# Optimization experiments

Hardware: AMD Instinct MI355X
Metric: run time of the kernel (lower is better)

## Reference

```python
import jax, jax.numpy as jnp
import numpy as np

B, H, S, D = 4, 16, 2048, 64


def setup_inputs() -> dict:
    key = jax.random.key(0)
    kq, kk, kv = jax.random.split(key, 3)
    q = jax.random.normal(kq, (B, H, S, D), dtype=jnp.float32)
    k = jax.random.normal(kk, (B, H, S, D), dtype=jnp.float32)
    v = jax.random.normal(kv, (B, H, S, D), dtype=jnp.float32)
    # causal mask, broadcastable over batch/heads (True = keep)
    mask = jnp.tril(jnp.ones((S, S), dtype=bool))[None, None, :, :]
    return {"q": q, "k": k, "v": v, "mask": mask}


def reference(q, k, v, mask):
    d_k = q.shape[-1]
    # [..., q, k] scores with full materialization, as in the original
    scores = jnp.einsum("bhqd,bhkd->bhqk", q, k) / jnp.sqrt(jnp.float32(d_k))
    scores = jnp.where(mask, scores, jnp.float32(-jnp.inf))
    attn = jax.nn.softmax(scores, axis=-1)  # stable: single max-subtract, matches manual softmax
    out = jnp.einsum("bhqk,bhkd->bhqd", attn, v)
    return out
```

## Files before the change

kernel.cpp:

```cpp
#include <hip/hip_runtime.h>
#include <hip/hip_bf16.h>
#include <stdint.h>

#define S_LEN 2048
#define D_DIM 64
#define BH    64
#define NQT   16
#define LOG2E 1.44269504088896f
#define THR   8.0f
#define TEN_ELEMS (BH * S_LEN * D_DIM)

typedef __attribute__((ext_vector_type(8)))  short bf16x8;
typedef __attribute__((ext_vector_type(4)))  short s16x4;
typedef __attribute__((ext_vector_type(4)))  float f32x4;
typedef __attribute__((ext_vector_type(16))) float f32x16;
typedef __attribute__((ext_vector_type(4)))  uint32_t u32x4;

__device__ __forceinline__ short f2bf(float f) {
    uint32_t u = __builtin_bit_cast(uint32_t, f);
    u += 0x7FFFu + ((u >> 16) & 1u);
    return (short)(u >> 16);
}

__device__ __forceinline__ uint32_t pkbf(float lo, float hi) {
    __hip_bfloat162 h = __float22bfloat162_rn(make_float2(lo, hi));
    uint32_t r;
    __builtin_memcpy(&r, &h, 4);
    return r;
}

__device__ __forceinline__ float xhalf_max(float v) {
    return fmaxf(v, __shfl_xor(v, 32));
}
__device__ __forceinline__ float xhalf_sum(float v) {
    return v + __shfl_xor(v, 32);
}

__device__ __forceinline__ int swz(int row, int col) {
    return (row * 64 + col) ^ ((row & 7) << 3);
}

#if __has_builtin(__builtin_amdgcn_exp2f)
#define EXP2(x) __builtin_amdgcn_exp2f(x)
#else
#define EXP2(x) exp2f(x)
#endif

__global__ __launch_bounds__(256)
void cvt_qk_kernel(const float* __restrict__ Q, const float* __restrict__ K,
                   short* __restrict__ Qb, short* __restrict__ Kb)
{
    const size_t off = ((size_t)blockIdx.x * 256 + threadIdx.x) * 8;
    const float sc = 0.125f * LOG2E;
    f32x4 a0 = *(const f32x4*)(Q + off), a1 = *(const f32x4*)(Q + off + 4);
    f32x4 b0 = *(const f32x4*)(K + off), b1 = *(const f32x4*)(K + off + 4);
    bf16x8 qa, kb;
    #pragma unroll
    for (int j = 0; j < 4; ++j) {
        qa[j] = f2bf(a0[j] * sc); qa[4 + j] = f2bf(a1[j] * sc);
        kb[j] = f2bf(b0[j]);      kb[4 + j] = f2bf(b1[j]);
    }
    *(bf16x8*)(Qb + off) = qa;
    *(bf16x8*)(Kb + off) = kb;
}

__global__ __launch_bounds__(256)
void vt_kernel(const float* __restrict__ V, short* __restrict__ Vt)
{
    const int kt = blockIdx.x;
    const int bh = blockIdx.y;
    const float* Vp = V + (size_t)bh * S_LEN * D_DIM + (size_t)kt * 64 * D_DIM;
    short* Vo = Vt + (size_t)bh * D_DIM * S_LEN;
    __shared__ short T[64][72];
    const int tid = threadIdx.x;
    const int row = tid >> 2, q4 = tid & 3;
    #pragma unroll
    for (int j = 0; j < 4; ++j) {
        f32x4 v = *(const f32x4*)(Vp + row * D_DIM + q4 * 16 + j * 4);
        #pragma unroll
        for (int e = 0; e < 4; ++e) T[row][q4 * 16 + j * 4 + e] = f2bf(v[e]);
    }
    __syncthreads();
    const int d = tid >> 2, kq = tid & 3;
    #pragma unroll
    for (int j = 0; j < 4; ++j) {
        s16x4 w;
        #pragma unroll
        for (int e = 0; e < 4; ++e) w[e] = T[kq * 16 + j * 4 + e][d];
        const int jd = (j == 1) ? 2 : ((j == 2) ? 1 : j);
        *(s16x4*)&Vo[(size_t)d * S_LEN + kt * 64 + kq * 16 + jd * 4] = w;
    }
}

#define ISSUE_B(kb) do { \
    const short* kp_ = Kp + (size_t)(kb) * 64 * D_DIM; \
    const short* vp_ = Vtp + (kb) * 64; \
    _Pragma("unroll") for (int it = 0; it < 4; ++it) { \
        const int idx_ = tid + it * 256; \
        const int row_ = idx_ >> 4, c4_ = idx_ & 15; \
        kreg[it] = *(const s16x4*)(kp_ + row_ * D_DIM + c4_ * 4); \
        vreg[it] = *(const s16x4*)(vp_ + (size_t)row_ * S_LEN + c4_ * 4); \
    } \
} while (0)

#define WRITE_LDS_B(b) do { \
    _Pragma("unroll") for (int it = 0; it < 4; ++it) { \
        const int idx_ = tid + it * 256; \
        const int row_ = idx_ >> 4, c4_ = idx_ & 15; \
        *(s16x4*)&Kl[b][swz(row_, c4_ * 4)] = kreg[it]; \
        *(s16x4*)&Vl[b][swz(row_, c4_ * 4)] = vreg[it]; \
    } \
} while (0)

#define MKFRAG(dst, sv, R0) do { \
    u32x4 t_; \
    t_[0] = pkbf(sv[(R0)+0], sv[(R0)+1]); \
    t_[1] = pkbf(sv[(R0)+2], sv[(R0)+3]); \
    t_[2] = pkbf(sv[(R0)+4], sv[(R0)+5]); \
    t_[3] = pkbf(sv[(R0)+6], sv[(R0)+7]); \
    dst = __builtin_bit_cast(bf16x8, t_); \
} while (0)

#define PVSTEP(pa, koff, acc0, acc1, b) do { \
    bf16x8 vf0_ = *(const bf16x8*)&Vl[b][swz(lq32,      (koff) + hi * 8)]; \
    bf16x8 vf1_ = *(const bf16x8*)&Vl[b][swz(32 + lq32, (koff) + hi * 8)]; \
    acc0 = __builtin_amdgcn_mfma_f32_32x32x16_bf16(pa, vf0_, acc0, 0, 0, 0); \
    acc1 = __builtin_amdgcn_mfma_f32_32x32x16_bf16(pa, vf1_, acc1, 0, 0, 0); \
} while (0)

#define COMPUTE32(qf, acc0, acc1, mm, ll, q0, kv0, b) do { \
    f32x16 s0_ = (f32x16)0.f, s1_ = (f32x16)0.f; \
    __builtin_amdgcn_s_setprio(1); \
    _Pragma("unroll") for (int c = 0; c < 4; ++c) { \
        bf16x8 k0_ = *(const bf16x8*)&Kl[b][swz(lq32,      c * 16 + hi * 8)]; \
        bf16x8 k1_ = *(const bf16x8*)&Kl[b][swz(32 + lq32, c * 16 + hi * 8)]; \
        s0_ = __builtin_amdgcn_mfma_f32_32x32x16_bf16(k0_, qf[c], s0_, 0, 0, 0); \
        s1_ = __builtin_amdgcn_mfma_f32_32x32x16_bf16(k1_, qf[c], s1_, 0, 0, 0); \
    } \
    __builtin_amdgcn_s_setprio(0); \
    if ((kv0) + 63 > (q0)) {    \
        _Pragma("unroll") for (int r = 0; r < 16; ++r) { \
            const int kvr_ = (r & 3) + 8 * (r >> 2) + 4 * hi; \
            if ((kv0) + kvr_      > (q0) + lq32) s0_[r] = -1e30f; \
            if ((kv0) + 32 + kvr_ > (q0) + lq32) s1_[r] = -1e30f; \
        } \
    } \
    float m0_ = fmaxf(s0_[0], s1_[0]), m1_ = fmaxf(s0_[1], s1_[1]); \
    float m2_ = fmaxf(s0_[2], s1_[2]), m3_ = fmaxf(s0_[3], s1_[3]); \
    _Pragma("unroll") for (int r = 4; r < 16; r += 4) { \
        m0_ = fmaxf(m0_, fmaxf(s0_[r],     s1_[r])); \
        m1_ = fmaxf(m1_, fmaxf(s0_[r + 1], s1_[r + 1])); \
        m2_ = fmaxf(m2_, fmaxf(s0_[r + 2], s1_[r + 2])); \
        m3_ = fmaxf(m3_, fmaxf(s0_[r + 3], s1_[r + 3])); \
    } \
    float pmax_ = xhalf_max(fmaxf(fmaxf(m0_, m1_), fmaxf(m2_, m3_))); \
    if (!__all(pmax_ <= (mm) + THR)) {       \
        const float mn_ = fmaxf((mm), pmax_); \
        const float f_  = EXP2((mm) - mn_); \
        (ll) *= f_; \
        _Pragma("unroll") for (int r = 0; r < 16; ++r) { \
            const float fr_ = __shfl(f_, (r & 3) + 8 * (r >> 2) + 4 * hi); \
            acc0[r] *= fr_; acc1[r] *= fr_; \
        } \
        (mm) = mn_; \
    } \
    float t0_ = 0.f, t1_ = 0.f, t2_ = 0.f, t3_ = 0.f; \
    _Pragma("unroll") for (int r = 0; r < 16; r += 4) { \
        s0_[r]     = EXP2(s0_[r]     - (mm)); s1_[r]     = EXP2(s1_[r]     - (mm)); \
        s0_[r + 1] = EXP2(s0_[r + 1] - (mm)); s1_[r + 1] = EXP2(s1_[r + 1] - (mm)); \
        s0_[r + 2] = EXP2(s0_[r + 2] - (mm)); s1_[r + 2] = EXP2(s1_[r + 2] - (mm)); \
        s0_[r + 3] = EXP2(s0_[r + 3] - (mm)); s1_[r + 3] = EXP2(s1_[r + 3] - (mm)); \
        t0_ += s0_[r]     + s1_[r]; \
        t1_ += s0_[r + 1] + s1_[r + 1]; \
        t2_ += s0_[r + 2] + s1_[r + 2]; \
        t3_ += s0_[r + 3] + s1_[r + 3]; \
    } \
    (ll) += (t0_ + t1_) + (t2_ + t3_);       \
    bf16x8 pa0_, pa1_, pa2_, pa3_; \
    MKFRAG(pa0_, s0_, 0); MKFRAG(pa1_, s0_, 8); \
    MKFRAG(pa2_, s1_, 0); MKFRAG(pa3_, s1_, 8); \
    __builtin_amdgcn_s_setprio(1); \
    PVSTEP(pa0_, 0,  acc0, acc1, b); \
    PVSTEP(pa1_, 16, acc0, acc1, b); \
    PVSTEP(pa2_, 32, acc0, acc1, b); \
    PVSTEP(pa3_, 48, acc0, acc1, b); \
    __builtin_amdgcn_s_setprio(0); \
} while (0)

__global__ __launch_bounds__(256, 2)
void attn_fwd_bf16(const short* __restrict__ Qb, const short* __restrict__ Kb,
                   const short* __restrict__ Vt, float* __restrict__ Out)
{
    const int bh   = blockIdx.x;
    const int qt   = NQT - 1 - blockIdx.y;
    const int tid  = threadIdx.x;
    const int wid  = tid >> 6;
    const int lane = tid & 63;
    const int lq32 = lane & 31;
    const int hi   = lane >> 5;

    const int nkv = 2 * qt + 2;

    const short* Qp  = Qb + (size_t)bh * S_LEN * D_DIM;
    const short* Kp  = Kb + (size_t)bh * S_LEN * D_DIM;
    const short* Vtp = Vt + (size_t)bh * D_DIM * S_LEN;
    float*       Op  = Out + (size_t)bh * S_LEN * D_DIM;

    __shared__ __align__(16) short Kl[2][64 * 64];
    __shared__ __align__(16) short Vl[2][64 * 64];

    const int q0 = qt * 128 + wid * 32;

    bf16x8 qf[4];
    #pragma unroll
    for (int c = 0; c < 4; ++c)
        qf[c] = *(const bf16x8*)(Qp + (size_t)(q0 + lq32) * D_DIM + c * 16 + hi * 8);

    f32x16 acc0 = (f32x16)0.f, acc1 = (f32x16)0.f;
    float m = -1e30f, l = 0.f;

    s16x4 kreg[4], vreg[4];

    ISSUE_B(0);
    WRITE_LDS_B(0);
    __syncthreads();

    for (int j = 0; j < nkv; ++j) {
        const int  kv0  = j * 64;
        const int  buf  = j & 1;
        const bool more = (j + 1) < nkv;
        if (more) ISSUE_B(j + 1);
        if (kv0 <= q0 + 31) COMPUTE32(qf, acc0, acc1, m, l, q0, kv0, buf);
        if (more) {
            WRITE_LDS_B(buf ^ 1);
            __syncthreads();
        }
    }

    l = xhalf_sum(l);
    const float il = 1.f / l;
    #pragma unroll
    for (int r = 0; r < 16; ++r) {
        const int qr   = (r & 3) + 8 * (r >> 2) + 4 * hi;
        const float vl = __shfl(il, qr);
        Op[(size_t)(q0 + qr) * D_DIM + lq32]      = acc0[r] * vl;
        Op[(size_t)(q0 + qr) * D_DIM + 32 + lq32] = acc1[r] * vl;
    }
}

extern "C" void kernel_launch(void* const* d_in, const int* in_sizes, int n_in,
                              void* d_out, int out_size, void* d_ws, size_t ws_size,
                              hipStream_t stream) {
    const float* q = (const float*)d_in[0];
    const float* k = (const float*)d_in[1];
    const float* v = (const float*)d_in[2];
    float* out = (float*)d_out;
    (void)in_sizes; (void)n_in; (void)out_size; (void)ws_size;

    short* Qb = (short*)d_ws;
    short* Kb = Qb + TEN_ELEMS;
    short* Vt = Kb + TEN_ELEMS;
    cvt_qk_kernel<<<TEN_ELEMS / 8 / 256, 256, 0, stream>>>(q, k, Qb, Kb);
    vt_kernel<<<dim3(S_LEN / 64, BH), 256, 0, stream>>>(v, Vt);
    attn_fwd_bf16<<<dim3(BH, NQT), 256, 0, stream>>>(Qb, Kb, Vt, out);
}
```

Before: 87.04 us.

## Software-pipeline QK of next tile with softmax/PV of current tile via triple buffering

Splits the per-tile attention step into a QK^T stage and a softmax+PV stage, and reorders the loop so the QK matmul for tile t+1 is issued before the softmax and PV of tile t. LDS K/V buffers go from two to three so the next tile can be written while the two live tiles are read. The aim is to overlap MFMA work with exp/max VALU work and hide LDS latency. In exchange it holds two extra f32x16 score registers per thread and uses more shared memory, which may cut occupancy at two blocks per CU.

```diff
diff --git a/kernel.cpp b/kernel.cpp
--- a/kernel.cpp
+++ b/kernel.cpp
@@ -103,12 +103,12 @@
     } \
 } while (0)
 
-#define WRITE_LDS_B(b) do { \
+#define WRITE_LDS_B(Kd_, Vd_) do { \
     _Pragma("unroll") for (int it = 0; it < 4; ++it) { \
         const int idx_ = tid + it * 256; \
         const int row_ = idx_ >> 4, c4_ = idx_ & 15; \
-        *(s16x4*)&Kl[b][swz(row_, c4_ * 4)] = kreg[it]; \
-        *(s16x4*)&Vl[b][swz(row_, c4_ * 4)] = vreg[it]; \
+        *(s16x4*)&(Kd_)[swz(row_, c4_ * 4)] = kreg[it]; \
+        *(s16x4*)&(Vd_)[swz(row_, c4_ * 4)] = vreg[it]; \
     } \
 } while (0)
 
@@ -121,30 +121,33 @@
     dst = __builtin_bit_cast(bf16x8, t_); \
 } while (0)
 
-#define PVSTEP(pa, koff, acc0, acc1, b) do { \
-    bf16x8 vf0_ = *(const bf16x8*)&Vl[b][swz(lq32,      (koff) + hi * 8)]; \
-    bf16x8 vf1_ = *(const bf16x8*)&Vl[b][swz(32 + lq32, (koff) + hi * 8)]; \
+#define PVSTEP(pa, koff, Vb_) do { \
+    bf16x8 vf0_ = *(const bf16x8*)&(Vb_)[swz(lq32,      (koff) + hi * 8)]; \
+    bf16x8 vf1_ = *(const bf16x8*)&(Vb_)[swz(32 + lq32, (koff) + hi * 8)]; \
     acc0 = __builtin_amdgcn_mfma_f32_32x32x16_bf16(pa, vf0_, acc0, 0, 0, 0); \
     acc1 = __builtin_amdgcn_mfma_f32_32x32x16_bf16(pa, vf1_, acc1, 0, 0, 0); \
 } while (0)
 
-#define COMPUTE32(qf, acc0, acc1, mm, ll, q0, kv0, b) do { \
-    f32x16 s0_ = (f32x16)0.f, s1_ = (f32x16)0.f; \
+#define QK32(sd0, sd1, kv0, Kb_) do { \
+    sd0 = (f32x16)0.f; sd1 = (f32x16)0.f; \
     __builtin_amdgcn_s_setprio(1); \
     _Pragma("unroll") for (int c = 0; c < 4; ++c) { \
-        bf16x8 k0_ = *(const bf16x8*)&Kl[b][swz(lq32,      c * 16 + hi * 8)]; \
-        bf16x8 k1_ = *(const bf16x8*)&Kl[b][swz(32 + lq32, c * 16 + hi * 8)]; \
-        s0_ = __builtin_amdgcn_mfma_f32_32x32x16_bf16(k0_, qf[c], s0_, 0, 0, 0); \
-        s1_ = __builtin_amdgcn_mfma_f32_32x32x16_bf16(k1_, qf[c], s1_, 0, 0, 0); \
+        bf16x8 k0_ = *(const bf16x8*)&(Kb_)[swz(lq32,      c * 16 + hi * 8)]; \
+        bf16x8 k1_ = *(const bf16x8*)&(Kb_)[swz(32 + lq32, c * 16 + hi * 8)]; \
+        sd0 = __builtin_amdgcn_mfma_f32_32x32x16_bf16(k0_, qf[c], sd0, 0, 0, 0); \
+        sd1 = __builtin_amdgcn_mfma_f32_32x32x16_bf16(k1_, qf[c], sd1, 0, 0, 0); \
     } \
     __builtin_amdgcn_s_setprio(0); \
-    if ((kv0) + 63 > (q0)) {    \
+    if ((kv0) + 63 > q0) { \
         _Pragma("unroll") for (int r = 0; r < 16; ++r) { \
             const int kvr_ = (r & 3) + 8 * (r >> 2) + 4 * hi; \
-            if ((kv0) + kvr_      > (q0) + lq32) s0_[r] = -1e30f; \
-            if ((kv0) + 32 + kvr_ > (q0) + lq32) s1_[r] = -1e30f; \
+            if ((kv0) + kvr_      > q0 + lq32) sd0[r] = -1e30f; \
+            if ((kv0) + 32 + kvr_ > q0 + lq32) sd1[r] = -1e30f; \
         } \
     } \
+} while (0)
+
+#define SMPV32(s0_, s1_, Vb_) do { \
     float m0_ = fmaxf(s0_[0], s1_[0]), m1_ = fmaxf(s0_[1], s1_[1]); \
     float m2_ = fmaxf(s0_[2], s1_[2]), m3_ = fmaxf(s0_[3], s1_[3]); \
     _Pragma("unroll") for (int r = 4; r < 16; r += 4) { \
@@ -154,36 +157,36 @@
         m3_ = fmaxf(m3_, fmaxf(s0_[r + 3], s1_[r + 3])); \
     } \
     float pmax_ = xhalf_max(fmaxf(fmaxf(m0_, m1_), fmaxf(m2_, m3_))); \
-    if (!__all(pmax_ <= (mm) + THR)) {       \
-        const float mn_ = fmaxf((mm), pmax_); \
-        const float f_  = EXP2((mm) - mn_); \
-        (ll) *= f_; \
+    if (!__all(pmax_ <= m + THR)) {       \
+        const float mn_ = fmaxf(m, pmax_); \
+        const float f_  = EXP2(m - mn_); \
+        l *= f_; \
         _Pragma("unroll") for (int r = 0; r < 16; ++r) { \
             const float fr_ = __shfl(f_, (r & 3) + 8 * (r >> 2) + 4 * hi); \
             acc0[r] *= fr_; acc1[r] *= fr_; \
         } \
-        (mm) = mn_; \
+        m = mn_; \
     } \
     float t0_ = 0.f, t1_ = 0.f, t2_ = 0.f, t3_ = 0.f; \
     _Pragma("unroll") for (int r = 0; r < 16; r += 4) { \
-        s0_[r]     = EXP2(s0_[r]     - (mm)); s1_[r]     = EXP2(s1_[r]     - (mm)); \
-        s0_[r + 1] = EXP2(s0_[r + 1] - (mm)); s1_[r + 1] = EXP2(s1_[r + 1] - (mm)); \
-        s0_[r + 2] = EXP2(s0_[r + 2] - (mm)); s1_[r + 2] = EXP2(s1_[r + 2] - (mm)); \
-        s0_[r + 3] = EXP2(s0_[r + 3] - (mm)); s1_[r + 3] = EXP2(s1_[r + 3] - (mm)); \
+        s0_[r]     = EXP2(s0_[r]     - m); s1_[r]     = EXP2(s1_[r]     - m); \
+        s0_[r + 1] = EXP2(s0_[r + 1] - m); s1_[r + 1] = EXP2(s1_[r + 1] - m); \
+        s0_[r + 2] = EXP2(s0_[r + 2] - m); s1_[r + 2] = EXP2(s1_[r + 2] - m); \
+        s0_[r + 3] = EXP2(s0_[r + 3] - m); s1_[r + 3] = EXP2(s1_[r + 3] - m); \
         t0_ += s0_[r]     + s1_[r]; \
         t1_ += s0_[r + 1] + s1_[r + 1]; \
         t2_ += s0_[r + 2] + s1_[r + 2]; \
         t3_ += s0_[r + 3] + s1_[r + 3]; \
     } \
-    (ll) += (t0_ + t1_) + (t2_ + t3_);       \
+    l += (t0_ + t1_) + (t2_ + t3_); \
     bf16x8 pa0_, pa1_, pa2_, pa3_; \
     MKFRAG(pa0_, s0_, 0); MKFRAG(pa1_, s0_, 8); \
     MKFRAG(pa2_, s1_, 0); MKFRAG(pa3_, s1_, 8); \
     __builtin_amdgcn_s_setprio(1); \
-    PVSTEP(pa0_, 0,  acc0, acc1, b); \
-    PVSTEP(pa1_, 16, acc0, acc1, b); \
-    PVSTEP(pa2_, 32, acc0, acc1, b); \
-    PVSTEP(pa3_, 48, acc0, acc1, b); \
+    PVSTEP(pa0_, 0,  Vb_); \
+    PVSTEP(pa1_, 16, Vb_); \
+    PVSTEP(pa2_, 32, Vb_); \
+    PVSTEP(pa3_, 48, Vb_); \
     __builtin_amdgcn_s_setprio(0); \
 } while (0)
 
@@ -206,10 +209,11 @@
     const short* Vtp = Vt + (size_t)bh * D_DIM * S_LEN;
     float*       Op  = Out + (size_t)bh * S_LEN * D_DIM;
 
-    __shared__ __align__(16) short Kl[2][64 * 64];
-    __shared__ __align__(16) short Vl[2][64 * 64];
-
-    const int q0 = qt * 128 + wid * 32;
+    __shared__ __align__(16) short Kl[3][64 * 64];
+    __shared__ __align__(16) short Vl[3][64 * 64];
+
+    const int q0   = qt * 128 + wid * 32;
+    const int Tmax = (q0 + 31) >> 6;
 
     bf16x8 qf[4];
     #pragma unroll
@@ -220,21 +224,31 @@
     float m = -1e30f, l = 0.f;
 
     s16x4 kreg[4], vreg[4];
+    f32x16 sA0, sA1, sB0, sB1;
 
     ISSUE_B(0);
-    WRITE_LDS_B(0);
+    WRITE_LDS_B(&Kl[0][0], &Vl[0][0]);
     __syncthreads();
-
-    for (int j = 0; j < nkv; ++j) {
-        const int  kv0  = j * 64;
-        const int  buf  = j & 1;
-        const bool more = (j + 1) < nkv;
-        if (more) ISSUE_B(j + 1);
-        if (kv0 <= q0 + 31) COMPUTE32(qf, acc0, acc1, m, l, q0, kv0, buf);
-        if (more) {
-            WRITE_LDS_B(buf ^ 1);
+    ISSUE_B(1);
+    QK32(sA0, sA1, 0, &Kl[0][0]);
+
+    for (int t = 0; t < nkv; t += 2) {
+        {
+            const int b1 = (t + 1) % 3;
+            WRITE_LDS_B(&Kl[b1][0], &Vl[b1][0]);
+            if (t + 2 < nkv) ISSUE_B(t + 2);
             __syncthreads();
+            if (t + 1 <= Tmax) QK32(sB0, sB1, 64 * (t + 1), &Kl[b1][0]);
+            if (t     <= Tmax) SMPV32(sA0, sA1, (&Vl[t % 3][0]));
         }
+        if (t + 2 < nkv) {
+            const int b2 = (t + 2) % 3;
+            WRITE_LDS_B(&Kl[b2][0], &Vl[b2][0]);
+            if (t + 3 < nkv) ISSUE_B(t + 3);
+            __syncthreads();
+            if (t + 2 <= Tmax) QK32(sA0, sA1, 64 * (t + 2), &Kl[b2][0]);
+        }
+        if (t + 1 <= Tmax) SMPV32(sB0, sB1, (&Vl[(t + 1) % 3][0]));
     }
 
     l = xhalf_sum(l);
```

Measured after the change: 95.83 us. 10.1% more time.

## Pre-swizzle K/V into tile images and stage them with direct global-to-LDS loads

Applied to the files above, without the earlier changes.

The conversion kernels now write K and transposed V as contiguous 64x64 bf16 tile images, already in the XOR-swizzled LDS layout. The attention kernel copies each tile straight into LDS with 16-byte global_load_lds instructions instead of loading into registers and then storing to LDS. This is meant to remove the register staging, the LDS store instructions and the strided V loads from the main loop, and to let the prefetch run asynchronously while compute proceeds. The cost is that correctness now depends on the compiler placing the right vmcnt waits before the barrier. The preprocessing kernels also gain more scattered write patterns.

```diff
diff --git a/kernel.cpp b/kernel.cpp
--- a/kernel.cpp
+++ b/kernel.cpp
@@ -46,11 +46,18 @@
 #define EXP2(x) exp2f(x)
 #endif
 
+typedef __attribute__((address_space(1))) const uint32_t glb_u32;
+typedef __attribute__((address_space(3))) uint32_t lds_u32;
+__device__ __forceinline__ void llds16(const short* g, short* l) {
+    __builtin_amdgcn_global_load_lds((glb_u32*)g, (lds_u32*)l, 16, 0, 0);
+}
+
 __global__ __launch_bounds__(256)
 void cvt_qk_kernel(const float* __restrict__ Q, const float* __restrict__ K,
-                   short* __restrict__ Qb, short* __restrict__ Kb)
+                   short* __restrict__ Qb, short* __restrict__ Kimg)
 {
-    const size_t off = ((size_t)blockIdx.x * 256 + threadIdx.x) * 8;
+    const size_t gid = (size_t)blockIdx.x * 256 + threadIdx.x;
+    const size_t off = gid * 8;
     const float sc = 0.125f * LOG2E;
     f32x4 a0 = *(const f32x4*)(Q + off), a1 = *(const f32x4*)(Q + off + 4);
     f32x4 b0 = *(const f32x4*)(K + off), b1 = *(const f32x4*)(K + off + 4);
@@ -61,16 +68,19 @@
         kb[j] = f2bf(b0[j]);      kb[4 + j] = f2bf(b1[j]);
     }
     *(bf16x8*)(Qb + off) = qa;
-    *(bf16x8*)(Kb + off) = kb;
+    const size_t s  = off >> 6;
+    const int    d0 = (int)(off & 63);
+    const int    row = (int)(s & 63);
+    *(bf16x8*)(Kimg + (s >> 6) * 4096 + swz(row, d0)) = kb;
 }
 
 __global__ __launch_bounds__(256)
-void vt_kernel(const float* __restrict__ V, short* __restrict__ Vt)
+void vt_kernel(const float* __restrict__ V, short* __restrict__ Vimg)
 {
     const int kt = blockIdx.x;
     const int bh = blockIdx.y;
     const float* Vp = V + (size_t)bh * S_LEN * D_DIM + (size_t)kt * 64 * D_DIM;
-    short* Vo = Vt + (size_t)bh * D_DIM * S_LEN;
+    short* Vo = Vimg + ((size_t)bh * 32 + kt) * 4096;
     __shared__ short T[64][72];
     const int tid = threadIdx.x;
     const int row = tid >> 2, q4 = tid & 3;
@@ -88,28 +98,18 @@
         #pragma unroll
         for (int e = 0; e < 4; ++e) w[e] = T[kq * 16 + j * 4 + e][d];
         const int jd = (j == 1) ? 2 : ((j == 2) ? 1 : j);
-        *(s16x4*)&Vo[(size_t)d * S_LEN + kt * 64 + kq * 16 + jd * 4] = w;
-    }
-}
-
-#define ISSUE_B(kb) do { \
-    const short* kp_ = Kp + (size_t)(kb) * 64 * D_DIM; \
-    const short* vp_ = Vtp + (kb) * 64; \
-    _Pragma("unroll") for (int it = 0; it < 4; ++it) { \
-        const int idx_ = tid + it * 256; \
-        const int row_ = idx_ >> 4, c4_ = idx_ & 15; \
-        kreg[it] = *(const s16x4*)(kp_ + row_ * D_DIM + c4_ * 4); \
-        vreg[it] = *(const s16x4*)(vp_ + (size_t)row_ * S_LEN + c4_ * 4); \
-    } \
-} while (0)
-
-#define WRITE_LDS_B(b) do { \
-    _Pragma("unroll") for (int it = 0; it < 4; ++it) { \
-        const int idx_ = tid + it * 256; \
-        const int row_ = idx_ >> 4, c4_ = idx_ & 15; \
-        *(s16x4*)&Kl[b][swz(row_, c4_ * 4)] = kreg[it]; \
-        *(s16x4*)&Vl[b][swz(row_, c4_ * 4)] = vreg[it]; \
-    } \
+        *(s16x4*)&Vo[swz(d, kq * 16 + jd * 4)] = w;
+    }
+}
+
+#define STAGE(kb, buf) do { \
+    const short* ks_ = Kimg + ((size_t)bh * 32 + (kb)) * 4096; \
+    const short* vs_ = Vimg + ((size_t)bh * 32 + (kb)) * 4096; \
+    const int wo_ = wid * 1024; \
+    llds16(ks_ + wo_ + lane * 8,       &Kl[buf][wo_]); \
+    llds16(ks_ + wo_ + 512 + lane * 8, &Kl[buf][wo_ + 512]); \
+    llds16(vs_ + wo_ + lane * 8,       &Vl[buf][wo_]); \
+    llds16(vs_ + wo_ + 512 + lane * 8, &Vl[buf][wo_ + 512]); \
 } while (0)
 
 #define MKFRAG(dst, sv, R0) do { \
@@ -188,8 +188,8 @@
 } while (0)
 
 __global__ __launch_bounds__(256, 2)
-void attn_fwd_bf16(const short* __restrict__ Qb, const short* __restrict__ Kb,
-                   const short* __restrict__ Vt, float* __restrict__ Out)
+void attn_fwd_bf16(const short* __restrict__ Qb, const short* __restrict__ Kimg,
+                   const short* __restrict__ Vimg, float* __restrict__ Out)
 {
     const int bh   = blockIdx.x;
     const int qt   = NQT - 1 - blockIdx.y;
@@ -201,10 +201,8 @@
 
     const int nkv = 2 * qt + 2;
 
-    const short* Qp  = Qb + (size_t)bh * S_LEN * D_DIM;
-    const short* Kp  = Kb + (size_t)bh * S_LEN * D_DIM;
-    const short* Vtp = Vt + (size_t)bh * D_DIM * S_LEN;
-    float*       Op  = Out + (size_t)bh * S_LEN * D_DIM;
+    const short* Qp = Qb + (size_t)bh * S_LEN * D_DIM;
+    float*       Op = Out + (size_t)bh * S_LEN * D_DIM;
 
     __shared__ __align__(16) short Kl[2][64 * 64];
     __shared__ __align__(16) short Vl[2][64 * 64];
@@ -219,22 +217,15 @@
     f32x16 acc0 = (f32x16)0.f, acc1 = (f32x16)0.f;
     float m = -1e30f, l = 0.f;
 
-    s16x4 kreg[4], vreg[4];
-
-    ISSUE_B(0);
-    WRITE_LDS_B(0);
+    STAGE(0, 0);
     __syncthreads();
 
     for (int j = 0; j < nkv; ++j) {
-        const int  kv0  = j * 64;
         const int  buf  = j & 1;
         const bool more = (j + 1) < nkv;
-        if (more) ISSUE_B(j + 1);
-        if (kv0 <= q0 + 31) COMPUTE32(qf, acc0, acc1, m, l, q0, kv0, buf);
-        if (more) {
-            WRITE_LDS_B(buf ^ 1);
-            __syncthreads();
-        }
+        if (more) STAGE(j + 1, buf ^ 1);
+        if (j * 64 <= q0 + 31) COMPUTE32(qf, acc0, acc1, m, l, q0, j * 64, buf);
+        if (more) __syncthreads();
     }
 
     l = xhalf_sum(l);
@@ -257,10 +248,10 @@
     float* out = (float*)d_out;
     (void)in_sizes; (void)n_in; (void)out_size; (void)ws_size;
 
-    short* Qb = (short*)d_ws;
-    short* Kb = Qb + TEN_ELEMS;
-    short* Vt = Kb + TEN_ELEMS;
-    cvt_qk_kernel<<<TEN_ELEMS / 8 / 256, 256, 0, stream>>>(q, k, Qb, Kb);
-    vt_kernel<<<dim3(S_LEN / 64, BH), 256, 0, stream>>>(v, Vt);
-    attn_fwd_bf16<<<dim3(BH, NQT), 256, 0, stream>>>(Qb, Kb, Vt, out);
-}
+    short* Qb   = (short*)d_ws;
+    short* Kimg = Qb + TEN_ELEMS;
+    short* Vimg = Kimg + TEN_ELEMS;
+    cvt_qk_kernel<<<TEN_ELEMS / 8 / 256, 256, 0, stream>>>(q, k, Qb, Kimg);
+    vt_kernel<<<dim3(S_LEN / 64, BH), 256, 0, stream>>>(v, Vimg);
+    attn_fwd_bf16<<<dim3(BH, NQT), 256, 0, stream>>>(Qb, Kimg, Vimg, out);
+}
```

New measurement: 89.27 us. 2.6% more time.
